# Kernel tuning notes

Measured on AMD Instinct MI355X. Metric: run time of the kernel, lower is better.

Reference implementation:

```python
import jax, jax.numpy as jnp
import numpy as np

B, H, W, C = 4, 64, 64, 256

def setup_inputs() -> dict:
    key = jax.random.key(0)
    k1, k2 = jax.random.split(key)
    xa = jax.random.normal(k1, (B, H, W, C), dtype=jnp.float32)
    xb = jax.random.normal(k2, (B, H, W, C), dtype=jnp.float32)
    gamma = jnp.float32(1.0)  # learned scalar (init 'zeros' in source; nonzero for testing)
    return {"xa": xa, "xb": xb, "gamma": gamma}


def _cross_branch(x_q, x_k, gamma):
    # x_q: source of queries, values, and residual; x_k: source of keys.
    b, h, w, c = x_q.shape
    q = x_q.reshape(b, h * w, c)            # [B,N,C]
    k = x_k.reshape(b, h * w, c)            # [B,N,C]
    energy = jnp.einsum('bnc,bmc->bnm', q, k)   # full N x N scores
    # softmax(max_row - energy) == softmax(-energy) (row max is shift-invariant)
    attention = jax.nn.softmax(-energy, axis=-1)
    out = jnp.einsum('bnm,bmc->bnc', attention, q)  # proj_value == reshaped x_q
    out = out.reshape(b, h, w, c)
    return gamma * out + x_q


def reference(xa, xb, gamma):
    out_a = _cross_branch(xa, xb, gamma)  # energya = Qa Kb^T, values/residual = xa
    out_b = _cross_branch(xb, xa, gamma)  # energyb = Qb Ka^T, values/residual = xb
    return (out_a, out_b)
```

## Files before the change

kernel.cpp:

```cpp
#include <hip/hip_runtime.h>
#include <hip/hip_bf16.h>
#include <stdint.h>

typedef _Float16 f16x8 __attribute__((ext_vector_type(8)));
typedef float f32x4 __attribute__((ext_vector_type(4)));

#define MFMA_F16(A, B, C) __builtin_amdgcn_mfma_f32_16x16x32_f16(A, B, C, 0, 0, 0)
#define GLOAD_LDS16(g, l)                                                     \
    __builtin_amdgcn_global_load_lds(                                         \
        (const __attribute__((address_space(1))) void*)(g),                   \
        (__attribute__((address_space(3))) void*)(l), 16, 0, 0)

constexpr int Bb = 4, Nn = 4096, Cc = 256;
constexpr int BQ = 128;
constexpr int BK = 64;
constexpr int NT = Nn / BK;
constexpr int KPAD = 256;
constexpr int VPAD = 64;
constexpr int PPAD = 72;

constexpr size_t ASZ = (size_t)2 * Bb * Nn * Cc;
constexpr size_t WS_NEED = ASZ * 2 * 3;

__global__ __launch_bounds__(256)
void prep_kernel(const float* __restrict__ xa, const float* __restrict__ xb,
                 _Float16* __restrict__ hi, _Float16* __restrict__ lo,
                 _Float16* __restrict__ vt)
{
    const int n0 = blockIdx.x * 64, c0 = blockIdx.y * 64, ib = blockIdx.z;
    const float* x = ((ib >> 2) == 0 ? xa : xb) + (size_t)(ib & 3) * Nn * Cc;
    const size_t base = (size_t)ib * Nn * Cc;
    __shared__ ushort tile[64][68];
    const int t = threadIdx.x;
    const int r0 = t >> 4;
    const int c4 = (t & 15) * 4;
    #pragma unroll
    for (int ii = 0; ii < 4; ++ii) {
        const int r = r0 + ii * 16;
        float4 v = *(const float4*)&x[(size_t)(n0 + r) * Cc + c0 + c4];
        float vv[4] = {v.x, v.y, v.z, v.w};
        union { _Float16 h[4]; uint2 q; } H, L;
        #pragma unroll
        for (int e = 0; e < 4; ++e) {
            _Float16 h = (_Float16)vv[e];
            H.h[e] = h;
            L.h[e] = (_Float16)(vv[e] - (float)h);
        }
        *(uint2*)&hi[base + (size_t)(n0 + r) * Cc + c0 + c4] = H.q;
        *(uint2*)&lo[base + (size_t)(n0 + r) * Cc + c0 + c4] = L.q;
        *(uint2*)&tile[r][c4] = H.q;
    }
    __syncthreads();
    const int j4 = (t & 15) * 4;
    #pragma unroll
    for (int ii = 0; ii < 4; ++ii) {
        const int cr = r0 + ii * 16;
        ushort4 o;
        o.x = tile[j4 + 0][cr]; o.y = tile[j4 + 1][cr];
        o.z = tile[j4 + 2][cr]; o.w = tile[j4 + 3][cr];
        *(ushort4*)&vt[base + (size_t)(c0 + cr) * Nn + n0 + j4] = o;
    }
}

template<bool PREP>
__global__ __launch_bounds__(512, 1)
void attn_kernel(const float* __restrict__ xa, const float* __restrict__ xb,
                 const float* __restrict__ gamma_p, float* __restrict__ out,
                 const _Float16* __restrict__ hi, const _Float16* __restrict__ lo,
                 const _Float16* __restrict__ vt)
{
    const int qtile = blockIdx.x, b = blockIdx.y, dir = blockIdx.z;
    const float* qsrc = (dir == 0 ? xa : xb) + (size_t)b * Nn * Cc;
    const float* ksrc = (dir == 0 ? xb : xa) + (size_t)b * Nn * Cc;
    float* outp = out + (size_t)dir * Bb * Nn * Cc + (size_t)b * Nn * Cc;
    const int qib = dir * Bb + b;
    const int kib = (dir ^ 1) * Bb + b;
    const _Float16* qhiB = hi + (size_t)qib * Nn * Cc;
    const _Float16* qloB = lo + (size_t)qib * Nn * Cc;
    const _Float16* kB   = hi + (size_t)kib * Nn * Cc;
    const _Float16* vtB  = vt + (size_t)qib * Nn * Cc;

    __shared__ _Float16 sK[2][BK][KPAD];
    __shared__ _Float16 sVt[2][Cc][VPAD];
    __shared__ _Float16 sP[8][16][PPAD];

    const int t = threadIdx.x, lane = t & 63, w = t >> 6;
    const int l15 = lane & 15, g = lane >> 4;
    const int khalf = g * 8;
    const int rsw = (l15 & 7) << 3;

    f16x8 qhi[8], qlo[8];
    const int qrow = qtile * BQ + w * 16 + l15;
    if constexpr (PREP) {
        #pragma unroll
        for (int j = 0; j < 8; ++j) {
            union { uint4 u; f16x8 h; } A, C2;
            A.u  = *(const uint4*)(qhiB + (size_t)qrow * Cc + j * 32 + khalf);
            C2.u = *(const uint4*)(qloB + (size_t)qrow * Cc + j * 32 + khalf);
            A.u.x ^= 0x80008000u; A.u.y ^= 0x80008000u; A.u.z ^= 0x80008000u; A.u.w ^= 0x80008000u;
            C2.u.x ^= 0x80008000u; C2.u.y ^= 0x80008000u; C2.u.z ^= 0x80008000u; C2.u.w ^= 0x80008000u;
            qhi[j] = A.h; qlo[j] = C2.h;
        }
    } else {
        const float* qb = qsrc + (size_t)qrow * Cc;
        #pragma unroll
        for (int j = 0; j < 8; ++j) {
            float4 v0 = *(const float4*)(qb + j * 32 + khalf);
            float4 v1 = *(const float4*)(qb + j * 32 + khalf + 4);
            float xv[8] = {v0.x, v0.y, v0.z, v0.w, v1.x, v1.y, v1.z, v1.w};
            #pragma unroll
            for (int e = 0; e < 8; ++e) {
                float xn = -xv[e];
                _Float16 h = (_Float16)xn;
                qhi[j][e] = h;
                qlo[j][e] = (_Float16)(xn - (float)h);
            }
        }
    }

    f32x4 O[16];
    #pragma unroll
    for (int i = 0; i < 16; ++i) O[i] = (f32x4){0.f, 0.f, 0.f, 0.f};
    float mrow[4] = {-INFINITY, -INFINITY, -INFINITY, -INFINITY};
    float lsum[4] = {0.f, 0.f, 0.f, 0.f};

    const int krow0 = w * 8;
    const int klsub = lane >> 5;
    int offK[4];
    #pragma unroll
    for (int i = 0; i < 4; ++i) {
        const int rsub = i * 2 + klsub;
        const int sc = ((lane & 31) * 8) ^ ((rsub & 7) << 3);
        offK[i] = (krow0 + rsub) * Cc + sc;
    }
    const int vrow0 = w * 32;
    const int vlsub = lane >> 3;
    const int vcol  = ((lane & 7) * 8) ^ ((vlsub & 7) << 3);
    int offV[4];
    #pragma unroll
    for (int i = 0; i < 4; ++i)
        offV[i] = (vrow0 + i * 8 + vlsub) * Nn + vcol;

    auto stage = [&](int bufi, int m0) {
        #pragma unroll
        for (int i = 0; i < 4; ++i)
            GLOAD_LDS16(kB + (size_t)m0 * Cc + offK[i], &sK[bufi][krow0 + i * 2][0]);
        #pragma unroll
        for (int i = 0; i < 4; ++i)
            GLOAD_LDS16(vtB + (size_t)m0 + offV[i], &sVt[bufi][vrow0 + i * 8][0]);
    };

    auto compute = [&](int cur) {
        f32x4 S[4];
        #pragma unroll
        for (int s = 0; s < 4; ++s) S[s] = (f32x4){0.f, 0.f, 0.f, 0.f};
        __builtin_amdgcn_s_setprio(1);
        #pragma unroll
        for (int j = 0; j < 8; ++j) {
            const int ko = j * 32 + khalf;
            f16x8 k0 = *(const f16x8*)&sK[cur][l15][ko ^ rsw];
            f16x8 k1 = *(const f16x8*)&sK[cur][16 + l15][ko ^ rsw];
            f16x8 k2 = *(const f16x8*)&sK[cur][32 + l15][ko ^ rsw];
            f16x8 k3 = *(const f16x8*)&sK[cur][48 + l15][ko ^ rsw];
            S[0] = MFMA_F16(qhi[j], k0, S[0]);
            S[1] = MFMA_F16(qhi[j], k1, S[1]);
            S[2] = MFMA_F16(qhi[j], k2, S[2]);
            S[3] = MFMA_F16(qhi[j], k3, S[3]);
            S[0] = MFMA_F16(qlo[j], k0, S[0]);
            S[1] = MFMA_F16(qlo[j], k1, S[1]);
            S[2] = MFMA_F16(qlo[j], k2, S[2]);
            S[3] = MFMA_F16(qlo[j], k3, S[3]);
        }
        __builtin_amdgcn_s_setprio(0);

        float tmax4[4];
        bool need = false;
        #pragma unroll
        for (int r = 0; r < 4; ++r) {
            float tm = fmaxf(fmaxf(S[0][r], S[1][r]), fmaxf(S[2][r], S[3][r]));
            #pragma unroll
            for (int off = 8; off >= 1; off >>= 1)
                tm = fmaxf(tm, __shfl_xor(tm, off, 64));
            tmax4[r] = tm;
            need = need || (tm > mrow[r] + 8.f);
        }
        if (__any(need)) {
            float a4[4];
            #pragma unroll
            for (int r = 0; r < 4; ++r) {
                float mn = fmaxf(mrow[r], tmax4[r]);
                a4[r] = __expf(mrow[r] - mn);
                mrow[r] = mn;
                lsum[r] *= a4[r];
            }
            #pragma unroll
            for (int i = 0; i < 16; ++i) {
                #pragma unroll
                for (int r = 0; r < 4; ++r) O[i][r] *= a4[r];
            }
        }
        const int prow = g * 4;
        #pragma unroll
        for (int r = 0; r < 4; ++r) {
            float ps = 0.f;
            #pragma unroll
            for (int s = 0; s < 4; ++s) {
                float p = __expf(S[s][r] - mrow[r]);
                ps += p;
                sP[w][prow + r][s * 16 + l15] = (_Float16)p;
            }
            lsum[r] += ps;
        }
        asm volatile("s_waitcnt lgkmcnt(0)" ::: "memory");
        __builtin_amdgcn_sched_barrier(0);

        f16x8 pa0 = *(const f16x8*)&sP[w][l15][khalf];
        f16x8 pa1 = *(const f16x8*)&sP[w][l15][32 + khalf];
        __builtin_amdgcn_s_setprio(1);
        #pragma unroll
        for (int i = 0; i < 16; ++i) {
            f16x8 vb0 = *(const f16x8*)&sVt[cur][i * 16 + l15][khalf ^ rsw];
            f16x8 vb1 = *(const f16x8*)&sVt[cur][i * 16 + l15][(32 + khalf) ^ rsw];
            O[i] = MFMA_F16(pa0, vb0, O[i]);
            O[i] = MFMA_F16(pa1, vb1, O[i]);
        }
        __builtin_amdgcn_s_setprio(0);
    };

    if constexpr (PREP) {
        stage(0, 0);
        __syncthreads();
        for (int ti = 0; ti < NT; ++ti) {
            if (ti + 1 < NT) stage((ti & 1) ^ 1, (ti + 1) * BK);
            compute(ti & 1);
            __syncthreads();
        }
    } else {
        const int fr = t & 63, fc = (t >> 6) * 32;
        const int fsw = (fr & 7) << 3;
        for (int ti = 0; ti < NT; ++ti) {
            const int m0 = ti * BK;
            __syncthreads();
            #pragma unroll
            for (int e = 0; e < 32; e += 4) {
                float4 kv = *(const float4*)&ksrc[(size_t)(m0 + fr) * Cc + fc + e];
                sK[0][fr][(fc + e + 0) ^ fsw] = (_Float16)kv.x;
                sK[0][fr][(fc + e + 1) ^ fsw] = (_Float16)kv.y;
                sK[0][fr][(fc + e + 2) ^ fsw] = (_Float16)kv.z;
                sK[0][fr][(fc + e + 3) ^ fsw] = (_Float16)kv.w;
                float4 xv = *(const float4*)&qsrc[(size_t)(m0 + fr) * Cc + fc + e];
                sVt[0][fc + e + 0][fr ^ (((fc + e + 0) & 7) << 3)] = (_Float16)xv.x;
                sVt[0][fc + e + 1][fr ^ (((fc + e + 1) & 7) << 3)] = (_Float16)xv.y;
                sVt[0][fc + e + 2][fr ^ (((fc + e + 2) & 7) << 3)] = (_Float16)xv.z;
                sVt[0][fc + e + 3][fr ^ (((fc + e + 3) & 7) << 3)] = (_Float16)xv.w;
            }
            __syncthreads();
            compute(0);
        }
    }

    const float gma = gamma_p[0];
    #pragma unroll
    for (int r = 0; r < 4; ++r) {
        float lv = lsum[r];
        #pragma unroll
        for (int off = 8; off >= 1; off >>= 1)
            lv += __shfl_xor(lv, off, 64);
        const float inv = 1.f / lv;
        const int row = qtile * BQ + w * 16 + g * 4 + r;
        const size_t ro = (size_t)row * Cc + l15;
        #pragma unroll
        for (int i = 0; i < 16; ++i) {
            float o = O[i][r] * inv;
            outp[ro + i * 16] = gma * o + qsrc[ro + i * 16];
        }
    }
}

extern "C" void kernel_launch(void* const* d_in, const int* in_sizes, int n_in,
                              void* d_out, int out_size, void* d_ws, size_t ws_size,
                              hipStream_t stream) {
    (void)in_sizes; (void)n_in; (void)out_size;
    const float* xa = (const float*)d_in[0];
    const float* xb = (const float*)d_in[1];
    const float* gm = (const float*)d_in[2];
    float* out = (float*)d_out;

    dim3 agrid(Nn / BQ, Bb, 2);
    if (ws_size >= WS_NEED) {
        _Float16* hi = (_Float16*)d_ws;
        _Float16* lo = hi + ASZ;
        _Float16* vt = lo + ASZ;
        prep_kernel<<<dim3(Nn / 64, Cc / 64, 2 * Bb), 256, 0, stream>>>(xa, xb, hi, lo, vt);
        attn_kernel<true><<<agrid, 512, 0, stream>>>(xa, xb, gm, out, hi, lo, vt);
    } else {
        attn_kernel<false><<<agrid, 512, 0, stream>>>(xa, xb, gm, out, nullptr, nullptr, nullptr);
    }
}
```

Before: 243.2 us.

## Read V directly from global memory and remap blocks for L2 sharing

Drops the LDS staging buffer for the transposed V tile. The PV MFMA loop now loads its B-operands straight from the global transposed fp16 array, and the fallback path does strided fp32 global reads. The grid is flattened to 1D with batch and direction in the low bits, so blocks that run at the same time use different batches and directions but the same q-tile index. The aim is to save LDS and cut staging work, but each wave now issues uncached-layout global loads inside the inner loop, with extra latency and redundant traffic across waves.

Measured after the change: 621.9 us. 2.56x slower.

```diff
diff --git a/kernel.cpp b/kernel.cpp
--- a/kernel.cpp
+++ b/kernel.cpp
@@ -16,7 +16,6 @@
 constexpr int BK = 64;
 constexpr int NT = Nn / BK;
 constexpr int KPAD = 256;
-constexpr int VPAD = 64;
 constexpr int PPAD = 72;
 
 constexpr size_t ASZ = (size_t)2 * Bb * Nn * Cc;
@@ -69,7 +68,8 @@
                  const _Float16* __restrict__ hi, const _Float16* __restrict__ lo,
                  const _Float16* __restrict__ vt)
 {
-    const int qtile = blockIdx.x, b = blockIdx.y, dir = blockIdx.z;
+    const int bid = blockIdx.x;
+    const int qtile = bid >> 3, b = bid & 3, dir = (bid >> 2) & 1;
     const float* qsrc = (dir == 0 ? xa : xb) + (size_t)b * Nn * Cc;
     const float* ksrc = (dir == 0 ? xb : xa) + (size_t)b * Nn * Cc;
     float* outp = out + (size_t)dir * Bb * Nn * Cc + (size_t)b * Nn * Cc;
@@ -81,7 +81,6 @@
     const _Float16* vtB  = vt + (size_t)qib * Nn * Cc;
 
     __shared__ _Float16 sK[2][BK][KPAD];
-    __shared__ _Float16 sVt[2][Cc][VPAD];
     __shared__ _Float16 sP[8][16][PPAD];
 
     const int t = threadIdx.x, lane = t & 63, w = t >> 6;
@@ -133,24 +132,13 @@
         const int sc = ((lane & 31) * 8) ^ ((rsub & 7) << 3);
         offK[i] = (krow0 + rsub) * Cc + sc;
     }
-    const int vrow0 = w * 32;
-    const int vlsub = lane >> 3;
-    const int vcol  = ((lane & 7) * 8) ^ ((vlsub & 7) << 3);
-    int offV[4];
-    #pragma unroll
-    for (int i = 0; i < 4; ++i)
-        offV[i] = (vrow0 + i * 8 + vlsub) * Nn + vcol;
-
     auto stage = [&](int bufi, int m0) {
         #pragma unroll
         for (int i = 0; i < 4; ++i)
             GLOAD_LDS16(kB + (size_t)m0 * Cc + offK[i], &sK[bufi][krow0 + i * 2][0]);
-        #pragma unroll
-        for (int i = 0; i < 4; ++i)
-            GLOAD_LDS16(vtB + (size_t)m0 + offV[i], &sVt[bufi][vrow0 + i * 8][0]);
     };
 
-    auto compute = [&](int cur) {
+    auto compute = [&](int cur, int m0) {
         f32x4 S[4];
         #pragma unroll
         for (int s = 0; s < 4; ++s) S[s] = (f32x4){0.f, 0.f, 0.f, 0.f};
@@ -217,12 +205,28 @@
         f16x8 pa0 = *(const f16x8*)&sP[w][l15][khalf];
         f16x8 pa1 = *(const f16x8*)&sP[w][l15][32 + khalf];
         __builtin_amdgcn_s_setprio(1);
-        #pragma unroll
-        for (int i = 0; i < 16; ++i) {
-            f16x8 vb0 = *(const f16x8*)&sVt[cur][i * 16 + l15][khalf ^ rsw];
-            f16x8 vb1 = *(const f16x8*)&sVt[cur][i * 16 + l15][(32 + khalf) ^ rsw];
-            O[i] = MFMA_F16(pa0, vb0, O[i]);
-            O[i] = MFMA_F16(pa1, vb1, O[i]);
+        if constexpr (PREP) {
+            const _Float16* vg = vtB + (size_t)l15 * Nn + m0 + khalf;
+            #pragma unroll
+            for (int i = 0; i < 16; ++i) {
+                f16x8 vb0 = *(const f16x8*)(vg + (size_t)i * 16 * Nn);
+                f16x8 vb1 = *(const f16x8*)(vg + (size_t)i * 16 * Nn + 32);
+                O[i] = MFMA_F16(pa0, vb0, O[i]);
+                O[i] = MFMA_F16(pa1, vb1, O[i]);
+            }
+        } else {
+            #pragma unroll
+            for (int i = 0; i < 16; ++i) {
+                f16x8 vb0, vb1;
+                const int c = i * 16 + l15;
+                #pragma unroll
+                for (int e = 0; e < 8; ++e) {
+                    vb0[e] = (_Float16)qsrc[(size_t)(m0 + khalf + e) * Cc + c];
+                    vb1[e] = (_Float16)qsrc[(size_t)(m0 + 32 + khalf + e) * Cc + c];
+                }
+                O[i] = MFMA_F16(pa0, vb0, O[i]);
+                O[i] = MFMA_F16(pa1, vb1, O[i]);
+            }
         }
         __builtin_amdgcn_s_setprio(0);
     };
@@ -232,7 +236,7 @@
         __syncthreads();
         for (int ti = 0; ti < NT; ++ti) {
             if (ti + 1 < NT) stage((ti & 1) ^ 1, (ti + 1) * BK);
-            compute(ti & 1);
+            compute(ti & 1, ti * BK);
             __syncthreads();
         }
     } else {
@@ -248,14 +252,9 @@
                 sK[0][fr][(fc + e + 1) ^ fsw] = (_Float16)kv.y;
                 sK[0][fr][(fc + e + 2) ^ fsw] = (_Float16)kv.z;
                 sK[0][fr][(fc + e + 3) ^ fsw] = (_Float16)kv.w;
-                float4 xv = *(const float4*)&qsrc[(size_t)(m0 + fr) * Cc + fc + e];
-                sVt[0][fc + e + 0][fr ^ (((fc + e + 0) & 7) << 3)] = (_Float16)xv.x;
-                sVt[0][fc + e + 1][fr ^ (((fc + e + 1) & 7) << 3)] = (_Float16)xv.y;
-                sVt[0][fc + e + 2][fr ^ (((fc + e + 2) & 7) << 3)] = (_Float16)xv.z;
-                sVt[0][fc + e + 3][fr ^ (((fc + e + 3) & 7) << 3)] = (_Float16)xv.w;
             }
             __syncthreads();
-            compute(0);
+            compute(0, m0);
         }
     }
 
@@ -286,7 +285,7 @@
     const float* gm = (const float*)d_in[2];
     float* out = (float*)d_out;
 
-    dim3 agrid(Nn / BQ, Bb, 2);
+    dim3 agrid(256);
     if (ws_size >= WS_NEED) {
         _Float16* hi = (_Float16*)d_ws;
         _Float16* lo = hi + ASZ;
```

## Compute transposed scores and redistribute P through lane shuffles instead of LDS

Applied to the files above, without the earlier changes.

Swaps the MFMA operand order so each lane holds one query row's scores. Row max and row sum then reduce with two cross-group shuffles instead of four per-row butterfly reductions. The probability tile is packed to fp16 with cvt_pkrtz and rearranged into the PV A-operand layout using cross-lane shuffles and selects, which removes the sP LDS round trip and its waitcnt barrier. The grid is also flattened to 1D with a new block-to-(qtile, batch, direction) mapping. The cost is more shuffle and select instructions per tile and a more intricate register permutation that has to be exactly right.

After: 218.4 us. 1.11x faster.

```diff
diff --git a/kernel.cpp b/kernel.cpp
--- a/kernel.cpp
+++ b/kernel.cpp
@@ -3,6 +3,7 @@
 #include <stdint.h>
 
 typedef _Float16 f16x8 __attribute__((ext_vector_type(8)));
+typedef __fp16 fp16x2_t __attribute__((ext_vector_type(2)));
 typedef float f32x4 __attribute__((ext_vector_type(4)));
 
 #define MFMA_F16(A, B, C) __builtin_amdgcn_mfma_f32_16x16x32_f16(A, B, C, 0, 0, 0)
@@ -17,10 +18,15 @@
 constexpr int NT = Nn / BK;
 constexpr int KPAD = 256;
 constexpr int VPAD = 64;
-constexpr int PPAD = 72;
 
 constexpr size_t ASZ = (size_t)2 * Bb * Nn * Cc;
 constexpr size_t WS_NEED = ASZ * 2 * 3;
+
+__device__ __forceinline__ uint32_t pk16(float a, float b) {
+    union { fp16x2_t h; uint32_t u; } cv;
+    cv.h = __builtin_amdgcn_cvt_pkrtz(a, b);
+    return cv.u;
+}
 
 __global__ __launch_bounds__(256)
 void prep_kernel(const float* __restrict__ xa, const float* __restrict__ xb,
@@ -69,7 +75,8 @@
                  const _Float16* __restrict__ hi, const _Float16* __restrict__ lo,
                  const _Float16* __restrict__ vt)
 {
-    const int qtile = blockIdx.x, b = blockIdx.y, dir = blockIdx.z;
+    const int bid = blockIdx.x;
+    const int qtile = bid >> 3, b = bid & 3, dir = (bid >> 2) & 1;
     const float* qsrc = (dir == 0 ? xa : xb) + (size_t)b * Nn * Cc;
     const float* ksrc = (dir == 0 ? xb : xa) + (size_t)b * Nn * Cc;
     float* outp = out + (size_t)dir * Bb * Nn * Cc + (size_t)b * Nn * Cc;
@@ -82,7 +89,6 @@
 
     __shared__ _Float16 sK[2][BK][KPAD];
     __shared__ _Float16 sVt[2][Cc][VPAD];
-    __shared__ _Float16 sP[8][16][PPAD];
 
     const int t = threadIdx.x, lane = t & 63, w = t >> 6;
     const int l15 = lane & 15, g = lane >> 4;
@@ -121,8 +127,8 @@
     f32x4 O[16];
     #pragma unroll
     for (int i = 0; i < 16; ++i) O[i] = (f32x4){0.f, 0.f, 0.f, 0.f};
-    float mrow[4] = {-INFINITY, -INFINITY, -INFINITY, -INFINITY};
-    float lsum[4] = {0.f, 0.f, 0.f, 0.f};
+    float mrow = -INFINITY;
+    float lsum = 0.f;
 
     const int krow0 = w * 8;
     const int klsub = lane >> 5;
@@ -162,60 +168,98 @@
             f16x8 k1 = *(const f16x8*)&sK[cur][16 + l15][ko ^ rsw];
             f16x8 k2 = *(const f16x8*)&sK[cur][32 + l15][ko ^ rsw];
             f16x8 k3 = *(const f16x8*)&sK[cur][48 + l15][ko ^ rsw];
-            S[0] = MFMA_F16(qhi[j], k0, S[0]);
-            S[1] = MFMA_F16(qhi[j], k1, S[1]);
-            S[2] = MFMA_F16(qhi[j], k2, S[2]);
-            S[3] = MFMA_F16(qhi[j], k3, S[3]);
-            S[0] = MFMA_F16(qlo[j], k0, S[0]);
-            S[1] = MFMA_F16(qlo[j], k1, S[1]);
-            S[2] = MFMA_F16(qlo[j], k2, S[2]);
-            S[3] = MFMA_F16(qlo[j], k3, S[3]);
+            S[0] = MFMA_F16(k0, qhi[j], S[0]);
+            S[1] = MFMA_F16(k1, qhi[j], S[1]);
+            S[2] = MFMA_F16(k2, qhi[j], S[2]);
+            S[3] = MFMA_F16(k3, qhi[j], S[3]);
+            S[0] = MFMA_F16(k0, qlo[j], S[0]);
+            S[1] = MFMA_F16(k1, qlo[j], S[1]);
+            S[2] = MFMA_F16(k2, qlo[j], S[2]);
+            S[3] = MFMA_F16(k3, qlo[j], S[3]);
         }
         __builtin_amdgcn_s_setprio(0);
 
-        float tmax4[4];
-        bool need = false;
-        #pragma unroll
-        for (int r = 0; r < 4; ++r) {
-            float tm = fmaxf(fmaxf(S[0][r], S[1][r]), fmaxf(S[2][r], S[3][r]));
-            #pragma unroll
-            for (int off = 8; off >= 1; off >>= 1)
-                tm = fmaxf(tm, __shfl_xor(tm, off, 64));
-            tmax4[r] = tm;
-            need = need || (tm > mrow[r] + 8.f);
-        }
+        float tm = fmaxf(fmaxf(fmaxf(S[0][0], S[0][1]), fmaxf(S[0][2], S[0][3])),
+                         fmaxf(fmaxf(S[1][0], S[1][1]), fmaxf(S[1][2], S[1][3])));
+        tm = fmaxf(tm, fmaxf(fmaxf(fmaxf(S[2][0], S[2][1]), fmaxf(S[2][2], S[2][3])),
+                             fmaxf(fmaxf(S[3][0], S[3][1]), fmaxf(S[3][2], S[3][3]))));
+        tm = fmaxf(tm, __shfl_xor(tm, 16, 64));
+        tm = fmaxf(tm, __shfl_xor(tm, 32, 64));
+        const bool need = tm > mrow + 8.f;
         if (__any(need)) {
-            float a4[4];
-            #pragma unroll
-            for (int r = 0; r < 4; ++r) {
-                float mn = fmaxf(mrow[r], tmax4[r]);
-                a4[r] = __expf(mrow[r] - mn);
-                mrow[r] = mn;
-                lsum[r] *= a4[r];
-            }
+            float mn = fmaxf(mrow, tm);
+            float a = __expf(mrow - mn);
+            mrow = mn;
+            lsum *= a;
+            const int base = lane & 48;
+            const int g4 = (g & 3) * 4;
+            float a0 = __shfl(a, base | (g4 + 0), 64);
+            float a1 = __shfl(a, base | (g4 + 1), 64);
+            float a2 = __shfl(a, base | (g4 + 2), 64);
+            float a3 = __shfl(a, base | (g4 + 3), 64);
             #pragma unroll
             for (int i = 0; i < 16; ++i) {
-                #pragma unroll
-                for (int r = 0; r < 4; ++r) O[i][r] *= a4[r];
+                O[i][0] *= a0; O[i][1] *= a1; O[i][2] *= a2; O[i][3] *= a3;
             }
         }
-        const int prow = g * 4;
-        #pragma unroll
-        for (int r = 0; r < 4; ++r) {
-            float ps = 0.f;
-            #pragma unroll
-            for (int s = 0; s < 4; ++s) {
-                float p = __expf(S[s][r] - mrow[r]);
-                ps += p;
-                sP[w][prow + r][s * 16 + l15] = (_Float16)p;
-            }
-            lsum[r] += ps;
-        }
-        asm volatile("s_waitcnt lgkmcnt(0)" ::: "memory");
-        __builtin_amdgcn_sched_barrier(0);
-
-        f16x8 pa0 = *(const f16x8*)&sP[w][l15][khalf];
-        f16x8 pa1 = *(const f16x8*)&sP[w][l15][32 + khalf];
+
+        uint32_t P2[4][2];
+        float ps = 0.f;
+        #pragma unroll
+        for (int s = 0; s < 4; ++s) {
+            float p0 = __expf(S[s][0] - mrow);
+            float p1 = __expf(S[s][1] - mrow);
+            float p2 = __expf(S[s][2] - mrow);
+            float p3 = __expf(S[s][3] - mrow);
+            ps += (p0 + p1) + (p2 + p3);
+            P2[s][0] = pk16(p0, p1);
+            P2[s][1] = pk16(p2, p3);
+        }
+        lsum += ps;
+
+        uint32_t q00 = __shfl_xor(P2[0][0], 16, 64);
+        uint32_t q01 = __shfl_xor(P2[0][1], 16, 64);
+        uint32_t q10 = __shfl_xor(P2[1][0], 16, 64);
+        uint32_t q11 = __shfl_xor(P2[1][1], 16, 64);
+        uint32_t q20 = __shfl_xor(P2[2][0], 16, 64);
+        uint32_t q21 = __shfl_xor(P2[2][1], 16, 64);
+        uint32_t q30 = __shfl_xor(P2[3][0], 16, 64);
+        uint32_t q31 = __shfl_xor(P2[3][1], 16, 64);
+        const bool low = (g < 2);
+        const bool odd = (g & 1);
+        uint32_t m0_ = low ? P2[1][0] : P2[0][0];
+        uint32_t m1_ = low ? P2[1][1] : P2[0][1];
+        uint32_t m2_ = low ? P2[3][0] : P2[2][0];
+        uint32_t m3_ = low ? P2[3][1] : P2[2][1];
+        uint32_t p0_ = low ? q10 : q00;
+        uint32_t p1_ = low ? q11 : q01;
+        uint32_t p2_ = low ? q30 : q20;
+        uint32_t p3_ = low ? q31 : q21;
+        uint32_t sl0 = odd ? p0_ : m0_, sh0 = odd ? m0_ : p0_;
+        uint32_t sl1 = odd ? p1_ : m1_, sh1 = odd ? m1_ : p1_;
+        uint32_t sl2 = odd ? p2_ : m2_, sh2 = odd ? m2_ : p2_;
+        uint32_t sl3 = odd ? p3_ : m3_, sh3 = odd ? m3_ : p3_;
+        uint32_t R0 = __shfl_xor(sl0, 32, 64);
+        uint32_t R1 = __shfl_xor(sl1, 32, 64);
+        uint32_t R2 = __shfl_xor(sl2, 32, 64);
+        uint32_t R3 = __shfl_xor(sl3, 32, 64);
+        uint32_t R4 = __shfl_xor(sh0, 32, 64);
+        uint32_t R5 = __shfl_xor(sh1, 32, 64);
+        uint32_t R6 = __shfl_xor(sh2, 32, 64);
+        uint32_t R7 = __shfl_xor(sh3, 32, 64);
+        uint32_t A0 = (g == 0) ? P2[0][0] : ((g == 3) ? q10 : R0);
+        uint32_t A1 = (g == 0) ? P2[0][1] : ((g == 3) ? q11 : R1);
+        uint32_t A2 = (g == 0) ? P2[2][0] : ((g == 3) ? q30 : R2);
+        uint32_t A3 = (g == 0) ? P2[2][1] : ((g == 3) ? q31 : R3);
+        uint32_t B0 = (g == 0) ? q00 : ((g == 3) ? P2[1][0] : R4);
+        uint32_t B1 = (g == 0) ? q01 : ((g == 3) ? P2[1][1] : R5);
+        uint32_t B2 = (g == 0) ? q20 : ((g == 3) ? P2[3][0] : R6);
+        uint32_t B3 = (g == 0) ? q21 : ((g == 3) ? P2[3][1] : R7);
+        union { uint32_t u[4]; f16x8 h; } U0, U1;
+        U0.u[0] = A0; U0.u[1] = A1; U0.u[2] = B0; U0.u[3] = B1;
+        U1.u[0] = A2; U1.u[1] = A3; U1.u[2] = B2; U1.u[3] = B3;
+        f16x8 pa0 = U0.h, pa1 = U1.h;
+
         __builtin_amdgcn_s_setprio(1);
         #pragma unroll
         for (int i = 0; i < 16; ++i) {
@@ -259,15 +303,17 @@
         }
     }
 
+    float lv = lsum;
+    lv += __shfl_xor(lv, 16, 64);
+    lv += __shfl_xor(lv, 32, 64);
     const float gma = gamma_p[0];
+    const int base = lane & 48;
+    const int g4 = (g & 3) * 4;
     #pragma unroll
     for (int r = 0; r < 4; ++r) {
-        float lv = lsum[r];
-        #pragma unroll
-        for (int off = 8; off >= 1; off >>= 1)
-            lv += __shfl_xor(lv, off, 64);
-        const float inv = 1.f / lv;
-        const int row = qtile * BQ + w * 16 + g * 4 + r;
+        const float lvr = __shfl(lv, base | (g4 + r), 64);
+        const float inv = 1.f / lvr;
+        const int row = qtile * BQ + w * 16 + g4 + r;
         const size_t ro = (size_t)row * Cc + l15;
         #pragma unroll
         for (int i = 0; i < 16; ++i) {
@@ -286,7 +332,7 @@
     const float* gm = (const float*)d_in[2];
     float* out = (float*)d_out;
 
-    dim3 agrid(Nn / BQ, Bb, 2);
+    dim3 agrid(256);
     if (ws_size >= WS_NEED) {
         _Float16* hi = (_Float16*)d_ws;
         _Float16* lo = hi + ASZ;
```
